# Kernel optimization log

Measured on AMD Instinct MI355X. Metric: run time of the kernel, lower is better.

Reference implementation:

```python
import jax, jax.numpy as jnp
import numpy as np

Q = 128      # number of slices
S = 8        # slice_length = C // Q = 1024 // 128
H = 32       # unit_dim[0]
BN_EPS = 1e-3  # Keras BatchNormalization default epsilon


def setup_inputs() -> dict:
    key = jax.random.key(0)
    ks = jax.random.split(key, 5)
    B = 32768
    x = jax.random.normal(ks[0], (B, 1, 1, Q * S), dtype=jnp.float32)
    # Per-slice (grouped) parameters for the q=128 independent MLPs.
    W1 = jax.random.normal(ks[1], (Q, S, H), dtype=jnp.float32) / np.sqrt(S)
    b1 = jnp.zeros((Q, H), dtype=jnp.float32)
    gamma = jnp.ones((Q, H), dtype=jnp.float32)
    beta = jnp.zeros((Q, H), dtype=jnp.float32)
    mov_mean = 0.1 * jax.random.normal(ks[2], (Q, H), dtype=jnp.float32)
    mov_var = jnp.ones((Q, H), dtype=jnp.float32) + 0.1 * jax.random.uniform(ks[3], (Q, H), dtype=jnp.float32)
    W2 = jax.random.normal(ks[4], (Q, H, 1), dtype=jnp.float32) / np.sqrt(H)
    b2 = jnp.zeros((Q, 1), dtype=jnp.float32)
    return {"x": x, "W1": W1, "b1": b1, "gamma": gamma, "beta": beta,
            "mov_mean": mov_mean, "mov_var": mov_var, "W2": W2, "b2": b2}


def reference(x, W1, b1, gamma, beta, mov_mean, mov_var, W2, b2):
    B = x.shape[0]
    xs = x.reshape(B, Q, -1)                       # (B, Q, S)
    # Grouped Dense(32) + ELU, all 128 slices in one batched matmul
    h = jnp.einsum('bqs,qsh->bqh', xs, W1) + b1    # (B, Q, H)
    h = jax.nn.elu(h)
    # BatchNormalization (inference: moving statistics)
    inv = gamma * jax.lax.rsqrt(mov_var + BN_EPS)  # (Q, H)
    h = (h - mov_mean) * inv + beta
    # Grouped Dense(1)
    out = jnp.einsum('bqh,qho->bqo', h, W2) + b2   # (B, Q, 1)
    return out[..., 0]                              # (B, Q)
```

## Files before the change

kernel.cpp:

```cpp
#include <hip/hip_runtime.h>
#include <hip/hip_bf16.h>


#define QN 128
#define SN 8
#define HN 32
#define XROW 1024
#define BN_EPS 1e-3f

typedef short bf16x8 __attribute__((ext_vector_type(8)));
typedef float f32x16 __attribute__((ext_vector_type(16)));
typedef unsigned int u32;

#define WS_A_BYTES   (QN * 64 * 16)
#define WS_W2P_OFF   WS_A_BYTES
#define WS_W2P_BYTES (QN * 32 * 4)
#define WS_B2P_OFF   (WS_W2P_OFF + WS_W2P_BYTES)

static __device__ __forceinline__ u32 pkbf(float lo, float hi) {
    union { __hip_bfloat162 h2; u32 u; } c;
    c.h2 = __float22bfloat162_rn(float2{lo, hi});
    return c.u;
}

__global__ void divenc_prep(const float* __restrict__ W1,
                            const float* __restrict__ b1,
                            const float* __restrict__ gamma_,
                            const float* __restrict__ beta_,
                            const float* __restrict__ mmean,
                            const float* __restrict__ mvar,
                            const float* __restrict__ W2,
                            const float* __restrict__ b2,
                            unsigned char* __restrict__ ws)
{
    const int q = blockIdx.x;
    const int m = threadIdx.x;

    u32 d0 = 0, d1 = 0, d2 = 0, d3 = 0;
    if (m < 32) {
        const int h = m;
        d0 = pkbf(W1[(q*SN + 0)*HN + h], W1[(q*SN + 1)*HN + h]);
        d1 = pkbf(W1[(q*SN + 2)*HN + h], W1[(q*SN + 3)*HN + h]);
        d2 = pkbf(W1[(q*SN + 4)*HN + h], W1[(q*SN + 5)*HN + h]);
        d3 = pkbf(W1[(q*SN + 6)*HN + h], W1[(q*SN + 7)*HN + h]);
    } else {
        const int h = m - 32;
        d0 = pkbf(b1[q*HN + h], 0.f);
    }
    ((uint4*)ws)[q*64 + m] = uint4{d0, d1, d2, d3};

    float* wsW2p = (float*)(ws + WS_W2P_OFF);
    float* wsB2p = (float*)(ws + WS_B2P_OFF);
    if (m < 32) {
        const int half = m >> 4, r = m & 15;
        const int h = (r & 3) + 8*(r >> 2) + 4*half;
        float inv = gamma_[q*HN+h] * rsqrtf(mvar[q*HN+h] + BN_EPS);
        wsW2p[q*32 + half*16 + r] = inv * W2[q*HN + h];
    }
    if (m == 0) {
        float acc = b2[q];
        for (int h = 0; h < HN; ++h) {
            float inv = gamma_[q*HN+h] * rsqrtf(mvar[q*HN+h] + BN_EPS);
            acc += (beta_[q*HN+h] - mmean[q*HN+h]*inv) * W2[q*HN+h];
        }
        wsB2p[q] = acc;
    }
}

__global__ __launch_bounds__(256, 4)
void divenc_mfma(const float* __restrict__ x,
                 const unsigned char* __restrict__ ws,
                 float* __restrict__ out)
{
    const int lane = threadIdx.x & 63;
    const int wv   = threadIdx.x >> 6;
    const int b0   = blockIdx.x * 64;
    const int qh   = blockIdx.y;
    const int half = lane >> 5;
    const int bl   = lane & 31;

    const uint4*  wsA  = (const uint4*)ws;
    const float*  wsW  = (const float*)(ws + WS_W2P_OFF);
    const float*  wsB2 = (const float*)(ws + WS_B2P_OFF);

    __shared__ float lds_out[64][65];

    const float* xrow = x + (size_t)(b0 + lane) * XROW;
    const u32 biasB = 0x00003F80u;

    for (int it = 0; it < 4; ++it) {
        const int qb = qh*64 + wv*16 + it*4;

        float4 xr[8];
        #pragma unroll
        for (int j = 0; j < 8; ++j)
            xr[j] = ((const float4*)(xrow + qb*SN))[j];

        u32 xb[16];
        #pragma unroll
        for (int j = 0; j < 8; ++j) {
            xb[2*j]   = pkbf(xr[j].x, xr[j].y);
            xb[2*j+1] = pkbf(xr[j].z, xr[j].w);
        }

        #pragma unroll
        for (int ql = 0; ql < 4; ++ql) {
            const int q      = qb + ql;
            const int qlocal = wv*16 + it*4 + ql;

            union { uint4 u; bf16x8 v; } A, B0, B1;
            A.u = wsA[q*64 + lane];

            const float* wp = wsW + q*32 + half*16;
            float w2r[16];
            #pragma unroll
            for (int r = 0; r < 16; ++r) w2r[r] = wp[r];
            const float b2p = wsB2[q];

            u32 bx0[4], bx1[4];
            #pragma unroll
            for (int d = 0; d < 4; ++d) {
                u32 own  = xb[ql*4 + d];
                u32 sw   = __shfl_xor(own, 32);
                u32 bias = (d == 0) ? biasB : 0u;
                bx0[d] = half ? bias : own;
                bx1[d] = half ? bias : sw;
            }
            B0.u = uint4{bx0[0], bx0[1], bx0[2], bx0[3]};
            B1.u = uint4{bx1[0], bx1[1], bx1[2], bx1[3]};

            f32x16 zero;
            #pragma unroll
            for (int r = 0; r < 16; ++r) zero[r] = 0.f;

            f32x16 dA = __builtin_amdgcn_mfma_f32_32x32x16_bf16(A.v, B0.v, zero, 0, 0, 0);
            float p0 = 0.f;
            #pragma unroll
            for (int r = 0; r < 16; ++r) {
                float z = dA[r];
                float e = __expf(fminf(z, 0.f)) - 1.f;
                p0 = fmaf(fmaxf(z, e), w2r[r], p0);
            }
            p0 += __shfl_xor(p0, 32);

            f32x16 dB = __builtin_amdgcn_mfma_f32_32x32x16_bf16(A.v, B1.v, zero, 0, 0, 0);
            float p1 = 0.f;
            #pragma unroll
            for (int r = 0; r < 16; ++r) {
                float z = dB[r];
                float e = __expf(fminf(z, 0.f)) - 1.f;
                p1 = fmaf(fmaxf(z, e), w2r[r], p1);
            }
            p1 += __shfl_xor(p1, 32);

            if (lane < 32) {
                lds_out[bl     ][qlocal] = p0 + b2p;
                lds_out[bl + 32][qlocal] = p1 + b2p;
            }
        }
    }

    __syncthreads();

    #pragma unroll
    for (int p = 0; p < 4; ++p) {
        const int row = wv*16 + p*4 + (lane >> 4);
        const int c0  = lane & 15;
        float* orow = out + (size_t)(b0 + row) * QN + qh*64;
        #pragma unroll
        for (int cc = 0; cc < 4; ++cc)
            orow[c0 + cc*16] = lds_out[row][c0 + cc*16];
    }
}

extern "C" void kernel_launch(void* const* d_in, const int* in_sizes, int n_in,
                              void* d_out, int out_size, void* d_ws, size_t ws_size,
                              hipStream_t stream) {
    const float* x      = (const float*)d_in[0];
    const float* W1     = (const float*)d_in[1];
    const float* b1     = (const float*)d_in[2];
    const float* gamma_ = (const float*)d_in[3];
    const float* beta_  = (const float*)d_in[4];
    const float* mmean  = (const float*)d_in[5];
    const float* mvar   = (const float*)d_in[6];
    const float* W2     = (const float*)d_in[7];
    const float* b2     = (const float*)d_in[8];
    float* out = (float*)d_out;
    unsigned char* ws = (unsigned char*)d_ws;

    const int Btot = in_sizes[0] / XROW;

    divenc_prep<<<QN, 64, 0, stream>>>(W1, b1, gamma_, beta_, mmean, mvar, W2, b2, ws);
    divenc_mfma<<<dim3(Btot / 64, 2), 256, 0, stream>>>(x, ws, out);
}
```

Baseline: 56.06 us.

## Restructure MFMA kernel: per-slice waves, bias in accumulator init, prefetched x tiles

The main kernel is reorganised so each of 8 waves owns one slice and walks 256 batch rows in four 64-row sub-tiles. The next sub-tile's x is prefetched while the current one runs. The b1 bias moves from an augmented B operand into the MFMA accumulator initial value, so every lane now carries real x data and the cross-half shuffles are gone. Outputs are staged in a double-buffered LDS slab and written as float4 per slice group. The costs are one __syncthreads per slice group, 512-thread blocks, and strided per-row x loads of only 32 bytes each.

Result: faster. 49.91 us (-11.0%).

```diff
diff --git a/kernel.cpp b/kernel.cpp
--- a/kernel.cpp
+++ b/kernel.cpp
@@ -12,10 +12,12 @@
 typedef float f32x16 __attribute__((ext_vector_type(16)));
 typedef unsigned int u32;
 
-#define WS_A_BYTES   (QN * 64 * 16)
-#define WS_W2P_OFF   WS_A_BYTES
-#define WS_W2P_BYTES (QN * 32 * 4)
-#define WS_B2P_OFF   (WS_W2P_OFF + WS_W2P_BYTES)
+#define WS_A_BYTES (QN * 64 * 16)
+#define WS_C_OFF   WS_A_BYTES
+#define WS_C_BYTES (QN * 32 * 4)
+#define WS_W_OFF   (WS_C_OFF + WS_C_BYTES)
+#define WS_W_BYTES (QN * 32 * 4)
+#define WS_B2_OFF  (WS_W_OFF + WS_W_BYTES)
 
 static __device__ __forceinline__ u32 pkbf(float lo, float hi) {
     union { __hip_bfloat162 h2; u32 u; } c;
@@ -23,14 +25,10 @@
     return c.u;
 }
 
-__global__ void divenc_prep(const float* __restrict__ W1,
-                            const float* __restrict__ b1,
-                            const float* __restrict__ gamma_,
-                            const float* __restrict__ beta_,
-                            const float* __restrict__ mmean,
-                            const float* __restrict__ mvar,
-                            const float* __restrict__ W2,
-                            const float* __restrict__ b2,
+__global__ void divenc_prep(const float* __restrict__ W1, const float* __restrict__ b1,
+                            const float* __restrict__ gamma_, const float* __restrict__ beta_,
+                            const float* __restrict__ mmean, const float* __restrict__ mvar,
+                            const float* __restrict__ W2, const float* __restrict__ b2,
                             unsigned char* __restrict__ ws)
 {
     const int q = blockIdx.x;
@@ -38,24 +36,22 @@
 
     u32 d0 = 0, d1 = 0, d2 = 0, d3 = 0;
     if (m < 32) {
-        const int h = m;
-        d0 = pkbf(W1[(q*SN + 0)*HN + h], W1[(q*SN + 1)*HN + h]);
-        d1 = pkbf(W1[(q*SN + 2)*HN + h], W1[(q*SN + 3)*HN + h]);
-        d2 = pkbf(W1[(q*SN + 4)*HN + h], W1[(q*SN + 5)*HN + h]);
-        d3 = pkbf(W1[(q*SN + 6)*HN + h], W1[(q*SN + 7)*HN + h]);
-    } else {
-        const int h = m - 32;
-        d0 = pkbf(b1[q*HN + h], 0.f);
+        d0 = pkbf(W1[(q*SN + 0)*HN + m], W1[(q*SN + 1)*HN + m]);
+        d1 = pkbf(W1[(q*SN + 2)*HN + m], W1[(q*SN + 3)*HN + m]);
+        d2 = pkbf(W1[(q*SN + 4)*HN + m], W1[(q*SN + 5)*HN + m]);
+        d3 = pkbf(W1[(q*SN + 6)*HN + m], W1[(q*SN + 7)*HN + m]);
     }
     ((uint4*)ws)[q*64 + m] = uint4{d0, d1, d2, d3};
 
-    float* wsW2p = (float*)(ws + WS_W2P_OFF);
-    float* wsB2p = (float*)(ws + WS_B2P_OFF);
+    float* wsC  = (float*)(ws + WS_C_OFF);
+    float* wsW  = (float*)(ws + WS_W_OFF);
+    float* wsB2 = (float*)(ws + WS_B2_OFF);
     if (m < 32) {
         const int half = m >> 4, r = m & 15;
         const int h = (r & 3) + 8*(r >> 2) + 4*half;
+        wsC[q*32 + m] = b1[q*HN + h];
         float inv = gamma_[q*HN+h] * rsqrtf(mvar[q*HN+h] + BN_EPS);
-        wsW2p[q*32 + half*16 + r] = inv * W2[q*HN + h];
+        wsW[q*32 + m] = inv * W2[q*HN + h];
     }
     if (m == 0) {
         float acc = b2[q];
@@ -63,113 +59,94 @@
             float inv = gamma_[q*HN+h] * rsqrtf(mvar[q*HN+h] + BN_EPS);
             acc += (beta_[q*HN+h] - mmean[q*HN+h]*inv) * W2[q*HN+h];
         }
-        wsB2p[q] = acc;
+        wsB2[q] = acc;
     }
 }
 
-__global__ __launch_bounds__(256, 4)
-void divenc_mfma(const float* __restrict__ x,
-                 const unsigned char* __restrict__ ws,
+__global__ __launch_bounds__(512, 4)
+void divenc_mfma(const float* __restrict__ x, const unsigned char* __restrict__ ws,
                  float* __restrict__ out)
 {
     const int lane = threadIdx.x & 63;
     const int wv   = threadIdx.x >> 6;
-    const int b0   = blockIdx.x * 64;
-    const int qh   = blockIdx.y;
     const int half = lane >> 5;
     const int bl   = lane & 31;
+    const int b0   = blockIdx.x * 256;
+    const int q0   = blockIdx.y * 32;
 
-    const uint4*  wsA  = (const uint4*)ws;
-    const float*  wsW  = (const float*)(ws + WS_W2P_OFF);
-    const float*  wsB2 = (const float*)(ws + WS_B2P_OFF);
+    const uint4* wsA  = (const uint4*)ws;
+    const float* wsC  = (const float*)(ws + WS_C_OFF);
+    const float* wsW  = (const float*)(ws + WS_W_OFF);
+    const float* wsB2 = (const float*)(ws + WS_B2_OFF);
 
-    __shared__ float lds_out[64][65];
+    __shared__ float slab[2][256][9];
 
-    const float* xrow = x + (size_t)(b0 + lane) * XROW;
-    const u32 biasB = 0x00003F80u;
+    #pragma unroll
+    for (int qg = 0; qg < 4; ++qg) {
+        const int q = q0 + qg*8 + wv;
 
-    for (int it = 0; it < 4; ++it) {
-        const int qb = qh*64 + wv*16 + it*4;
+        union { uint4 u; bf16x8 v; } A1, A2;
+        A1.u = wsA[q*64 + lane];
+        A2.u = wsA[q*64 + (lane ^ 32)];
 
-        float4 xr[8];
+        f32x16 cini;
+        const float* cp_ = wsC + q*32 + half*16;
         #pragma unroll
-        for (int j = 0; j < 8; ++j)
-            xr[j] = ((const float4*)(xrow + qb*SN))[j];
+        for (int r = 0; r < 16; ++r) cini[r] = cp_[r];
+        float w2r[16];
+        const float* wp_ = wsW + q*32 + half*16;
+        #pragma unroll
+        for (int r = 0; r < 16; ++r) w2r[r] = wp_[r];
+        const float b2p = wsB2[q];
 
-        u32 xb[16];
+        const float* xq = x + (size_t)b0 * XROW + q * SN;
+        float4 xa = *(const float4*)(xq + (size_t)lane * XROW);
+        float4 xc = *(const float4*)(xq + (size_t)lane * XROW + 4);
+
         #pragma unroll
-        for (int j = 0; j < 8; ++j) {
-            xb[2*j]   = pkbf(xr[j].x, xr[j].y);
-            xb[2*j+1] = pkbf(xr[j].z, xr[j].w);
+        for (int sub = 0; sub < 4; ++sub) {
+            const int nsub = (sub < 3) ? sub + 1 : sub;
+            const float* np = xq + (size_t)(nsub*64 + lane) * XROW;
+            float4 na = *(const float4*)np;
+            float4 nc = *(const float4*)(np + 4);
+
+            union { uint4 u; bf16x8 v; } B;
+            B.u = uint4{ pkbf(xa.x, xa.y), pkbf(xa.z, xa.w),
+                         pkbf(xc.x, xc.y), pkbf(xc.z, xc.w) };
+
+            f32x16 D0 = __builtin_amdgcn_mfma_f32_32x32x16_bf16(A1.v, B.v, cini, 0, 0, 0);
+            f32x16 D1 = __builtin_amdgcn_mfma_f32_32x32x16_bf16(A2.v, B.v, cini, 0, 0, 0);
+
+            float p0 = 0.f, p1 = 0.f;
+            #pragma unroll
+            for (int r = 0; r < 16; ++r) {
+                float z0 = D0[r];
+                float e0 = __expf(fminf(z0, 0.f)) - 1.f;
+                p0 = fmaf(fmaxf(z0, e0), w2r[r], p0);
+                float z1 = D1[r];
+                float e1 = __expf(fminf(z1, 0.f)) - 1.f;
+                p1 = fmaf(fmaxf(z1, e1), w2r[r], p1);
+            }
+            p0 += __shfl_xor(p0, 32);
+            p1 += __shfl_xor(p1, 32);
+
+            const float v = (half ? p1 : p0) + b2p;
+            slab[qg & 1][sub*64 + half*32 + bl][wv] = v;
+
+            xa = na; xc = nc;
         }
 
-        #pragma unroll
-        for (int ql = 0; ql < 4; ++ql) {
-            const int q      = qb + ql;
-            const int qlocal = wv*16 + it*4 + ql;
-
-            union { uint4 u; bf16x8 v; } A, B0, B1;
-            A.u = wsA[q*64 + lane];
-
-            const float* wp = wsW + q*32 + half*16;
-            float w2r[16];
-            #pragma unroll
-            for (int r = 0; r < 16; ++r) w2r[r] = wp[r];
-            const float b2p = wsB2[q];
-
-            u32 bx0[4], bx1[4];
-            #pragma unroll
-            for (int d = 0; d < 4; ++d) {
-                u32 own  = xb[ql*4 + d];
-                u32 sw   = __shfl_xor(own, 32);
-                u32 bias = (d == 0) ? biasB : 0u;
-                bx0[d] = half ? bias : own;
-                bx1[d] = half ? bias : sw;
-            }
-            B0.u = uint4{bx0[0], bx0[1], bx0[2], bx0[3]};
-            B1.u = uint4{bx1[0], bx1[1], bx1[2], bx1[3]};
-
-            f32x16 zero;
-            #pragma unroll
-            for (int r = 0; r < 16; ++r) zero[r] = 0.f;
-
-            f32x16 dA = __builtin_amdgcn_mfma_f32_32x32x16_bf16(A.v, B0.v, zero, 0, 0, 0);
-            float p0 = 0.f;
-            #pragma unroll
-            for (int r = 0; r < 16; ++r) {
-                float z = dA[r];
-                float e = __expf(fminf(z, 0.f)) - 1.f;
-                p0 = fmaf(fmaxf(z, e), w2r[r], p0);
-            }
-            p0 += __shfl_xor(p0, 32);
-
-            f32x16 dB = __builtin_amdgcn_mfma_f32_32x32x16_bf16(A.v, B1.v, zero, 0, 0, 0);
-            float p1 = 0.f;
-            #pragma unroll
-            for (int r = 0; r < 16; ++r) {
-                float z = dB[r];
-                float e = __expf(fminf(z, 0.f)) - 1.f;
-                p1 = fmaf(fmaxf(z, e), w2r[r], p1);
-            }
-            p1 += __shfl_xor(p1, 32);
-
-            if (lane < 32) {
-                lds_out[bl     ][qlocal] = p0 + b2p;
-                lds_out[bl + 32][qlocal] = p1 + b2p;
-            }
+        __syncthreads();
+        {
+            const int row = threadIdx.x >> 1;
+            const int cp  = (threadIdx.x & 1) * 4;
+            float4 vv;
+            vv.x = slab[qg & 1][row][cp + 0];
+            vv.y = slab[qg & 1][row][cp + 1];
+            vv.z = slab[qg & 1][row][cp + 2];
+            vv.w = slab[qg & 1][row][cp + 3];
+            *(float4*)(out + (size_t)(b0 + row) * QN + q0 + qg*8 + cp) = vv;
         }
-    }
-
-    __syncthreads();
-
-    #pragma unroll
-    for (int p = 0; p < 4; ++p) {
-        const int row = wv*16 + p*4 + (lane >> 4);
-        const int c0  = lane & 15;
-        float* orow = out + (size_t)(b0 + row) * QN + qh*64;
-        #pragma unroll
-        for (int cc = 0; cc < 4; ++cc)
-            orow[c0 + cc*16] = lds_out[row][c0 + cc*16];
     }
 }
 
@@ -191,5 +168,5 @@
     const int Btot = in_sizes[0] / XROW;
 
     divenc_prep<<<QN, 64, 0, stream>>>(W1, b1, gamma_, beta_, mmean, mvar, W2, b2, ws);
-    divenc_mfma<<<dim3(Btot / 64, 2), 256, 0, stream>>>(x, ws, out);
+    divenc_mfma<<<dim3(Btot / 256, QN / 32), 512, 0, stream>>>(x, ws, out);
 }
```
